# Kernel optimization log

Hardware: AMD Instinct MI355X
Metric: run time of the kernel (lower is better)

Reference implementation:

```python
import jax, jax.numpy as jnp
import numpy as np

EPS = 1e-06


def setup_inputs() -> dict:
    key = jax.random.key(0)
    k0, k1, k2, k3 = jax.random.split(key, 4)
    N = 4096  # num_gaussians (64**2)
    H = W = 128
    # Gaussian centers in [-1, 1]^2 (matches the init position grid range)
    position = jax.random.uniform(k0, (1, N, 2), minval=-1.0, maxval=1.0, dtype=jnp.float32)
    # Module stores color = raw_colors + 1 and subtracts 1 at the end of forward
    color = jax.random.uniform(k1, (1, N, 3), dtype=jnp.float32) + 1.0
    # Module init is log_scale = -5; use -3 +/- noise so kernels have visible support
    log_scale = jax.random.normal(k2, (1, N, 2), dtype=jnp.float32) * 0.5 - 3.0
    rotation = jax.random.normal(k3, (1, N), dtype=jnp.float32) * 0.5
    alphas = jnp.ones((1, N), dtype=jnp.float32)
    return dict(position=position, color=color, log_scale=log_scale,
                rotation=rotation, alphas=alphas, height=H, width=W, num_active=N)


def reference(position, color, log_scale, rotation, alphas, height, width, num_active):
    """2D anisotropic Gaussian splat render (dense per-pixel evaluation).

    For every pixel p and gaussian g: rotate the offset into the gaussian
    frame, evaluate exp(-0.5 * quadratic form), weight by alpha and
    accumulate color.  Output [1, 3, H, W] minus 1 (module returns render-1).
    """
    n = num_active
    pos = position[0, :n]                       # [N, 2]
    col = color[0, :n]                          # [N, 3]
    scale = jnp.exp(log_scale[0, :n]) + EPS     # [N, 2]
    rot = rotation[0, :n]                       # [N]
    alph = alphas[0, :n]                        # [N]

    # Pixel grid in [-1, 1], x along width, y along height
    xs = jnp.linspace(-1.0, 1.0, width, dtype=pos.dtype)
    ys = jnp.linspace(-1.0, 1.0, height, dtype=pos.dtype)
    x_grid, y_grid = jnp.meshgrid(xs, ys)       # each [H, W]
    P = height * width
    px = x_grid.reshape(P, 1)                   # [P, 1]
    py = y_grid.reshape(P, 1)

    dx = px - pos[None, :, 0]                   # [P, N]
    dy = py - pos[None, :, 1]                   # [P, N]
    c = jnp.cos(rot)[None, :]
    s = jnp.sin(rot)[None, :]
    u = dx * c + dy * s                         # rotated offsets [P, N]
    v = -dx * s + dy * c

    inv_sx = 1.0 / scale[:, 0][None, :]
    inv_sy = 1.0 / scale[:, 1][None, :]
    w = jnp.exp(-0.5 * ((u * inv_sx) ** 2 + (v * inv_sy) ** 2)) * alph[None, :]  # [P, N]

    img = jnp.einsum('pn,nc->pc', w, col)       # [P, 3]
    img = img.reshape(height, width, 3).transpose(2, 0, 1)[None]  # [1, 3, H, W]
    return img - 1.0
```

## Files before the change

kernel.cpp:

```cpp
#include <hip/hip_runtime.h>
#include <hip/hip_fp16.h>
#include <math.h>

#define EPSV 1e-6f
#define TPB 256
#define SLICES 32
#define PPT 4
#define GRP 2
#define GCAP 256

typedef float v2f __attribute__((ext_vector_type(2)));


__device__ __forceinline__ float pack_half2(float a, float b) {
    __half2 h = __floats2half2_rn(a, b);
    union { __half2 h; float f; } u; u.h = h;
    return u.f;
}

__global__ __launch_bounds__(TPB) void splat_fused(
        const float* __restrict__ pos,
        const float* __restrict__ col,
        const float* __restrict__ ls,
        const float* __restrict__ rot,
        const float* __restrict__ alph,
        const int* __restrict__ nact_p,
        const int* __restrict__ hptr,
        const int* __restrict__ wptr,
        float* __restrict__ partial,
        int N, int P, int g_per_slice) {
    __shared__ float4 sh[GCAP * 2];

    const int slice = blockIdx.y;
    const int t = threadIdx.x;

    int nact = *nact_p;
    for (int j = t; j < g_per_slice; j += TPB) {
        int g = slice * g_per_slice + j;
        float4 o0 = make_float4(0.f, 0.f, 0.f, 0.f);
        float4 o1 = o0;
        if (g < N && g < nact) {
            float sx = expf(ls[2 * g])     + EPSV;
            float sy = expf(ls[2 * g + 1]) + EPSV;
            float r  = rot[g];
            float c = cosf(r), s = sinf(r);
            const float K = 0.84932180028801904f;
            float iA =  K * c / sx;
            float iB =  K * s / sx;
            float iC = -K * s / sy;
            float iD =  K * c / sy;
            float px = pos[2 * g], py = pos[2 * g + 1];
            float E = -(iA * px + iB * py);
            float F = -(iC * px + iD * py);
            float a  = iA * iA + iC * iC;
            float b  = iB * iB + iD * iD;
            float cc = 2.0f * (iA * iB + iC * iD);
            float d  = 2.0f * (iA * E + iC * F);
            float e  = 2.0f * (iB * E + iD * F);
            float f  = E * E + F * F;
            float al = alph[g];
            float cr = al * col[3 * g];
            float cg = al * col[3 * g + 1];
            float cb = al * col[3 * g + 2];
            o0 = make_float4(-a, -b, -cc, -d);
            o1 = make_float4(-e, -f, pack_half2(cr, cg), pack_half2(cb, 0.f));
        }
        sh[2 * j]     = o0;
        sh[2 * j + 1] = o1;
    }
    __syncthreads();

    const int W = *wptr;
    const int H = *hptr;
    const int base = blockIdx.x * (TPB * PPT);
    v2f px2[GRP], py2[GRP], pxx2[GRP], pyy2[GRP], pxy2[GRP];
#pragma unroll
    for (int k = 0; k < GRP; ++k) {
#pragma unroll
        for (int e = 0; e < 2; ++e) {
            int p = base + t + (2 * k + e) * TPB;
            int x = (p < P) ? (p % W) : 0;
            int y = (p < P) ? (p / W) : 0;
            float fx = -1.0f + (float)x * (2.0f / (float)(W - 1));
            float fy = -1.0f + (float)y * (2.0f / (float)(H - 1));
            px2[k][e] = fx;  py2[k][e] = fy;
            pxx2[k][e] = fx * fx;  pyy2[k][e] = fy * fy;  pxy2[k][e] = fx * fy;
        }
    }

    v2f accr2[GRP], accg2[GRP], accb2[GRP];
#pragma unroll
    for (int k = 0; k < GRP; ++k) {
        accr2[k] = (v2f)(0.f); accg2[k] = (v2f)(0.f); accb2[k] = (v2f)(0.f);
    }

#pragma unroll 2
    for (int g = 0; g < g_per_slice; ++g) {
        float4 a0 = sh[2 * g];
        float4 a1 = sh[2 * g + 1];

        union { float f; __half2 h; } u01, u2x;
        u01.f = a1.z; u2x.f = a1.w;
        float cr = __low2float(u01.h);
        float cg = __high2float(u01.h);
        float cb = __low2float(u2x.h);

        v2f CA = {a0.x, a0.x}, CB = {a0.y, a0.y}, CC = {a0.z, a0.z};
        v2f CD = {a0.w, a0.w}, CE = {a1.x, a1.x}, CF = {a1.y, a1.y};
        v2f CR = {cr, cr}, CG = {cg, cg}, CBL = {cb, cb};

#pragma unroll
        for (int k = 0; k < GRP; ++k) {
            v2f tt = pxx2[k] * CA + CF;
            tt = pyy2[k] * CB + tt;
            tt = pxy2[k] * CC + tt;
            tt = px2[k]  * CD + tt;
            tt = py2[k]  * CE + tt;
            v2f w;
            w[0] = __builtin_amdgcn_exp2f(tt[0]);
            w[1] = __builtin_amdgcn_exp2f(tt[1]);
            accr2[k] = w * CR  + accr2[k];
            accg2[k] = w * CG  + accg2[k];
            accb2[k] = w * CBL + accb2[k];
        }
    }

    float* dst = partial + (size_t)slice * 3 * P;
#pragma unroll
    for (int k = 0; k < GRP; ++k) {
#pragma unroll
        for (int e = 0; e < 2; ++e) {
            int p = base + t + (2 * k + e) * TPB;
            if (p < P) {
                dst[p]         = accr2[k][e];
                dst[P + p]     = accg2[k][e];
                dst[2 * P + p] = accb2[k][e];
            }
        }
    }
}

__global__ __launch_bounds__(TPB) void splat_reduce(
        const float4* __restrict__ partial,
        float4* __restrict__ out,
        int total4) {
    int i = blockIdx.x * TPB + threadIdx.x;
    if (i >= total4) return;
    float4 s = make_float4(-1.f, -1.f, -1.f, -1.f);
#pragma unroll
    for (int sl = 0; sl < SLICES; ++sl) {
        float4 v = partial[(size_t)sl * total4 + i];
        s.x += v.x; s.y += v.y; s.z += v.z; s.w += v.w;
    }
    out[i] = s;
}

extern "C" void kernel_launch(void* const* d_in, const int* in_sizes, int n_in,
                              void* d_out, int out_size, void* d_ws, size_t ws_size,
                              hipStream_t stream) {
    const float* pos  = (const float*)d_in[0];
    const float* col  = (const float*)d_in[1];
    const float* ls   = (const float*)d_in[2];
    const float* rot  = (const float*)d_in[3];
    const float* alph = (const float*)d_in[4];
    const int*   hptr = (const int*)d_in[5];
    const int*   wptr = (const int*)d_in[6];
    const int*   nact = (const int*)d_in[7];

    int N = in_sizes[3];
    int P = out_size / 3;

    int g_per_slice = (N + SLICES - 1) / SLICES;
    if (g_per_slice > GCAP) g_per_slice = GCAP;

    float* partial = (float*)d_ws;

    int px_blocks = (P + TPB * PPT - 1) / (TPB * PPT);
    dim3 grid(px_blocks, SLICES);
    splat_fused<<<grid, TPB, 0, stream>>>(
        pos, col, ls, rot, alph, nact, hptr, wptr, partial, N, P, g_per_slice);

    int total4 = out_size / 4;
    splat_reduce<<<(total4 + TPB - 1) / TPB, TPB, 0, stream>>>(
        (const float4*)partial, (float4*)d_out, total4);
}
```

Measured before the change: 89.66 us.

## Fuse splat and slice reduction into one cooperative kernel with grid sync

Merges the splat kernel and the separate slice-reduction kernel into one cooperative launch. A grid-wide barrier follows the partial-sum writes, and the same blocks then reduce the 32 slices into the output. The aim is to drop the second kernel launch and its launch gap. In exchange it adds a grid-sync cost and requires the whole grid (16x32 = 512 blocks) to be co-resident. If the launch is rejected, no output is written.

```diff
diff --git a/kernel.cpp b/kernel.cpp
--- a/kernel.cpp
+++ b/kernel.cpp
@@ -1,4 +1,5 @@
 #include <hip/hip_runtime.h>
+#include <hip/hip_cooperative_groups.h>
 #include <hip/hip_fp16.h>
 #include <math.h>
 
@@ -18,7 +19,7 @@
     return u.f;
 }
 
-__global__ __launch_bounds__(TPB) void splat_fused(
+__global__ __launch_bounds__(TPB) void splat_coop(
         const float* __restrict__ pos,
         const float* __restrict__ col,
         const float* __restrict__ ls,
@@ -28,7 +29,8 @@
         const int* __restrict__ hptr,
         const int* __restrict__ wptr,
         float* __restrict__ partial,
-        int N, int P, int g_per_slice) {
+        float* __restrict__ out,
+        int N, int P, int g_per_slice, int total4) {
     __shared__ float4 sh[GCAP * 2];
 
     const int slice = blockIdx.y;
@@ -138,21 +140,22 @@
             }
         }
     }
-}
 
-__global__ __launch_bounds__(TPB) void splat_reduce(
-        const float4* __restrict__ partial,
-        float4* __restrict__ out,
-        int total4) {
-    int i = blockIdx.x * TPB + threadIdx.x;
-    if (i >= total4) return;
-    float4 s = make_float4(-1.f, -1.f, -1.f, -1.f);
+    __threadfence();
+    cooperative_groups::this_grid().sync();
+
+    int lin_block = blockIdx.y * gridDim.x + blockIdx.x;
+    int i = lin_block * TPB + t;
+    if (i < total4) {
+        const float4* p4 = (const float4*)partial;
+        float4 s = make_float4(-1.f, -1.f, -1.f, -1.f);
 #pragma unroll
-    for (int sl = 0; sl < SLICES; ++sl) {
-        float4 v = partial[(size_t)sl * total4 + i];
-        s.x += v.x; s.y += v.y; s.z += v.z; s.w += v.w;
+        for (int sl = 0; sl < SLICES; ++sl) {
+            float4 v = p4[(size_t)sl * total4 + i];
+            s.x += v.x; s.y += v.y; s.z += v.z; s.w += v.w;
+        }
+        ((float4*)out)[i] = s;
     }
-    out[i] = s;
 }
 
 extern "C" void kernel_launch(void* const* d_in, const int* in_sizes, int n_in,
@@ -174,13 +177,19 @@
     if (g_per_slice > GCAP) g_per_slice = GCAP;
 
     float* partial = (float*)d_ws;
+    float* out = (float*)d_out;
+    int total4 = out_size / 4;
 
     int px_blocks = (P + TPB * PPT - 1) / (TPB * PPT);
     dim3 grid(px_blocks, SLICES);
-    splat_fused<<<grid, TPB, 0, stream>>>(
-        pos, col, ls, rot, alph, nact, hptr, wptr, partial, N, P, g_per_slice);
+    dim3 block(TPB);
 
-    int total4 = out_size / 4;
-    splat_reduce<<<(total4 + TPB - 1) / TPB, TPB, 0, stream>>>(
-        (const float4*)partial, (float4*)d_out, total4);
+    void* args[] = {
+        (void*)&pos, (void*)&col, (void*)&ls, (void*)&rot, (void*)&alph,
+        (void*)&nact, (void*)&hptr, (void*)&wptr,
+        (void*)&partial, (void*)&out,
+        (void*)&N, (void*)&P, (void*)&g_per_slice, (void*)&total4,
+    };
+    hipLaunchCooperativeKernel((const void*)splat_coop, grid, block,
+                               args, 0, stream);
 }
```

After: 215.3 us. 2.4x slower.
